# Optimization experiments

Measured on AMD Instinct MI355X. Metric: run time of the kernel, lower is better.

Reference implementation:

```python
import jax, jax.numpy as jnp
import numpy as np

B, C, HW, P = 8, 128, 50176, 128  # batch, channels, flattened spatial, num parcels

def setup_inputs() -> dict:
    key = jax.random.key(0)
    k1, k2 = jax.random.split(key)
    x = jax.random.normal(k1, (B, C, HW), dtype=jnp.float32)
    # 0/1 parcel assignment mask [b, num_parcs, hw]
    parcel_mask_batch = jax.random.randint(k2, (B, P, HW), 0, 2).astype(jnp.float32)
    return {"x": x, "parcel_mask_batch": parcel_mask_batch}

def reference(x, parcel_mask_batch):
    # torch: for each i, x[i] @ mask[i].T  -> stacked [b, c, num_parcs]
    # out[b, c, p] = sum_hw x[b, c, hw] * mask[b, p, hw]
    return jnp.einsum('bch,bph->bcp', x, parcel_mask_batch)
```

## Files before the change

kernel.cpp:

```cpp
#include <hip/hip_runtime.h>
#include <hip/hip_bf16.h>

typedef float f32x4 __attribute__((ext_vector_type(4)));
typedef short short8 __attribute__((ext_vector_type(8)));

#define BATCH 8
#define CH    128
#define HWN   50176
#define PN    128
#define KSPLIT 64
#define KWIN  784
#define BK    64
#define NST   13

__device__ __forceinline__ ushort f2bf(float f){
  uint u = __float_as_uint(f);
  u += 0x7FFFu + ((u >> 16) & 1u);
  return (ushort)(u >> 16);
}
__device__ __forceinline__ float bf2f(ushort h){
  return __uint_as_float(((uint)h) << 16);
}

template<int EPI>
__global__ __launch_bounds__(256, 2)
void raggr_kernel(const float* __restrict__ X, const float* __restrict__ Mk,
                  float* __restrict__ OUT, float* __restrict__ PART){
  __shared__ char lds[49152];
  char* Xh = lds;
  char* Xl = lds + 16384;
  char* Mm = lds + 32768;

  const int tid  = threadIdx.x;
  const int b    = blockIdx.x >> 6;
  const int s    = blockIdx.x & 63;
  const int lane = tid & 63;
  const int wid  = tid >> 6;
  const int wrow = (wid >> 1) * 64;
  const int wcol = (wid & 1) * 64;

  const size_t base = (size_t)b * CH * HWN + (size_t)s * KWIN;
  const f32x4 z4 = {0.f, 0.f, 0.f, 0.f};

  f32x4 acc[4][4];
  #pragma unroll
  for(int m=0;m<4;++m)
    #pragma unroll
    for(int n=0;n<4;++n) acc[m][n] = z4;

  f32x4 xv[8], mv[8];

  #define ISSUE(tt) {                                                         \
    const int kv = (KWIN - (tt)*BK) < BK ? (KWIN - (tt)*BK) : BK;             \
    _Pragma("unroll")                                                         \
    for(int it=0; it<8; ++it){                                                \
      int f = it*256 + tid;                                                   \
      int row = f >> 4, kq = f & 15;                                          \
      bool ok = (kq*4) < kv;                                                  \
      size_t off = base + (size_t)row * HWN + (size_t)((tt)*BK + kq*4);       \
      size_t offc = ok ? off : base;                                          \
      f32x4 xt = *(const f32x4*)(X  + offc);                                  \
      f32x4 mt = *(const f32x4*)(Mk + offc);                                  \
      xv[it] = ok ? xt : z4;                                                  \
      mv[it] = ok ? mt : z4;                                                  \
    } }

  #define WRITE_LDS() {                                                       \
    _Pragma("unroll")                                                         \
    for(int it=0; it<8; ++it){                                                \
      int f = it*256 + tid;                                                   \
      int row = f >> 4, kq = f & 15;                                          \
      int boff = row*128 + ((kq*8) ^ ((row & 7) << 4));                       \
      ushort h0=f2bf(xv[it].x), h1=f2bf(xv[it].y),                            \
             h2=f2bf(xv[it].z), h3=f2bf(xv[it].w);                            \
      ushort l0=f2bf(xv[it].x - bf2f(h0)), l1=f2bf(xv[it].y - bf2f(h1)),      \
             l2=f2bf(xv[it].z - bf2f(h2)), l3=f2bf(xv[it].w - bf2f(h3));      \
      ushort m0=f2bf(mv[it].x), m1=f2bf(mv[it].y),                            \
             m2=f2bf(mv[it].z), m3=f2bf(mv[it].w);                            \
      uint2 uh; uh.x = (uint)h0 | ((uint)h1<<16); uh.y = (uint)h2 | ((uint)h3<<16); \
      uint2 ul; ul.x = (uint)l0 | ((uint)l1<<16); ul.y = (uint)l2 | ((uint)l3<<16); \
      uint2 um; um.x = (uint)m0 | ((uint)m1<<16); um.y = (uint)m2 | ((uint)m3<<16); \
      *(uint2*)(Xh + boff) = uh;                                              \
      *(uint2*)(Xl + boff) = ul;                                              \
      *(uint2*)(Mm + boff) = um;                                              \
    } }

  #define COMPUTE() {                                                         \
    _Pragma("unroll")                                                         \
    for(int ks=0; ks<2; ++ks){                                                \
      const int kb = ks*64 + ((lane >> 4) << 4);                              \
      short8 bfr[4], ah[4], al[4];                                            \
      _Pragma("unroll")                                                       \
      for(int n=0;n<4;++n){                                                   \
        int r = wcol + n*16 + (lane & 15);                                    \
        bfr[n] = *(const short8*)(Mm + r*128 + (kb ^ ((r&7)<<4)));            \
      }                                                                       \
      _Pragma("unroll")                                                       \
      for(int m=0;m<4;++m){                                                   \
        int r = wrow + m*16 + (lane & 15);                                    \
        int o = r*128 + (kb ^ ((r&7)<<4));                                    \
        ah[m] = *(const short8*)(Xh + o);                                     \
        al[m] = *(const short8*)(Xl + o);                                     \
      }                                                                       \
      _Pragma("unroll")                                                       \
      for(int m=0;m<4;++m)                                                    \
        _Pragma("unroll")                                                     \
        for(int n=0;n<4;++n){                                                 \
          acc[m][n] = __builtin_amdgcn_mfma_f32_16x16x32_bf16(ah[m], bfr[n], acc[m][n], 0,0,0); \
          acc[m][n] = __builtin_amdgcn_mfma_f32_16x16x32_bf16(al[m], bfr[n], acc[m][n], 0,0,0); \
        }                                                                     \
    } }

  ISSUE(0);
  WRITE_LDS();
  __syncthreads();

  #pragma unroll 1
  for(int t=0; t<NST; ++t){
    if(t+1 < NST) ISSUE(t+1);
    COMPUTE();
    __syncthreads();
    if(t+1 < NST){ WRITE_LDS(); __syncthreads(); }
  }

  if(EPI == 0){
    float* p = PART + ((size_t)(b*KSPLIT + s)) * 16384;
    #pragma unroll
    for(int m=0;m<4;++m){
      int row0 = wrow + m*16 + ((lane >> 4) << 2);
      #pragma unroll
      for(int n=0;n<4;++n){
        int col = wcol + n*16 + (lane & 15);
        #pragma unroll
        for(int j=0;j<4;++j) p[(size_t)(row0+j)*128 + col] = acc[m][n][j];
      }
    }
  } else {
    float* o = OUT + (size_t)b * 16384;
    #pragma unroll
    for(int m=0;m<4;++m){
      int row0 = wrow + m*16 + ((lane >> 4) << 2);
      #pragma unroll
      for(int n=0;n<4;++n){
        int col = wcol + n*16 + (lane & 15);
        #pragma unroll
        for(int j=0;j<4;++j) atomicAdd(&o[(size_t)(row0+j)*128 + col], acc[m][n][j]);
      }
    }
  }
}

__global__ void reduce_kernel(const float* __restrict__ PART, float* __restrict__ OUT){
  int idx = blockIdx.x * 256 + threadIdx.x;
  int b   = idx >> 12;
  int c4  = idx & 4095;
  const f32x4* p = (const f32x4*)PART;
  f32x4 sum = {0.f,0.f,0.f,0.f};
  size_t base_ = (size_t)b * KSPLIT * 4096 + (size_t)c4;
  #pragma unroll 8
  for(int s2=0; s2<KSPLIT; ++s2) sum += p[base_ + (size_t)s2*4096];
  ((f32x4*)OUT)[idx] = sum;
}

__global__ void zero_kernel(float* __restrict__ OUT){
  int idx = blockIdx.x * 256 + threadIdx.x;
  if(idx < BATCH*CH*PN) OUT[idx] = 0.f;
}

extern "C" void kernel_launch(void* const* d_in, const int* in_sizes, int n_in,
                              void* d_out, int out_size, void* d_ws, size_t ws_size,
                              hipStream_t stream){
  const float* X  = (const float*)d_in[0];
  const float* Mk = (const float*)d_in[1];
  float* O = (float*)d_out;

  const size_t part_bytes = (size_t)BATCH * KSPLIT * CH * PN * sizeof(float);
  if(ws_size >= part_bytes && d_ws != nullptr){
    float* part = (float*)d_ws;
    raggr_kernel<0><<<dim3(BATCH*KSPLIT), dim3(256), 0, stream>>>(X, Mk, O, part);
    reduce_kernel<<<dim3(128), dim3(256), 0, stream>>>(part, O);
  } else {
    zero_kernel<<<dim3(512), dim3(256), 0, stream>>>(O);
    raggr_kernel<1><<<dim3(BATCH*KSPLIT), dim3(256), 0, stream>>>(X, Mk, O, nullptr);
  }
}
```

Before: 428.1 us.

## Stage fp32 tiles via direct global-to-LDS loads with double buffering

Replaces the register-staged load, convert and LDS write path with global_load_lds DMA copies of raw fp32 tiles into double-buffered shared memory, cutting the K tile from 64 to 32 and removing one barrier per step. The bf16 hi/lo split of X and the mask conversion (now truncation) move to after the LDS read, inside the compute phase. A separate tail step handles the leftover 16 columns. This trades redundant per-wave conversion work and doubled fp32 LDS traffic for overlapped, register-free loading.

```diff
diff --git a/kernel.cpp b/kernel.cpp
--- a/kernel.cpp
+++ b/kernel.cpp
@@ -10,37 +10,69 @@
 #define PN    128
 #define KSPLIT 64
 #define KWIN  784
-#define BK    64
-#define NST   13
-
-__device__ __forceinline__ ushort f2bf(float f){
+#define BK    32
+#define NFULL 24
+#define TAILOFF (NFULL*BK)
+
+__device__ __forceinline__ ushort f2bf_rn(float f){
   uint u = __float_as_uint(f);
   u += 0x7FFFu + ((u >> 16) & 1u);
   return (ushort)(u >> 16);
 }
 __device__ __forceinline__ float bf2f(ushort h){
   return __uint_as_float(((uint)h) << 16);
+}
+
+__device__ __forceinline__ short8 cvt8_trunc(f32x4 a, f32x4 b){
+  union{ short8 v; ushort u[8]; } r;
+  r.u[0]=(ushort)(__float_as_uint(a.x)>>16); r.u[1]=(ushort)(__float_as_uint(a.y)>>16);
+  r.u[2]=(ushort)(__float_as_uint(a.z)>>16); r.u[3]=(ushort)(__float_as_uint(a.w)>>16);
+  r.u[4]=(ushort)(__float_as_uint(b.x)>>16); r.u[5]=(ushort)(__float_as_uint(b.y)>>16);
+  r.u[6]=(ushort)(__float_as_uint(b.z)>>16); r.u[7]=(ushort)(__float_as_uint(b.w)>>16);
+  return r.v;
+}
+
+__device__ __forceinline__ void cvt8_hilo(f32x4 a, f32x4 b, short8& h8, short8& l8){
+  union{ short8 v; ushort u[8]; } h, l;
+  float f[8] = {a.x,a.y,a.z,a.w,b.x,b.y,b.z,b.w};
+  #pragma unroll
+  for(int j=0;j<8;++j){
+    ushort hh = f2bf_rn(f[j]);
+    h.u[j] = hh;
+    l.u[j] = f2bf_rn(f[j] - bf2f(hh));
+  }
+  h8 = h.v; l8 = l.v;
+}
+
+__device__ __forceinline__ void gload16(const float* g, float* l){
+  __builtin_amdgcn_global_load_lds(
+      (const __attribute__((address_space(1))) void*)g,
+      (__attribute__((address_space(3))) void*)l, 16, 0, 0);
+}
+
+__device__ __forceinline__ f32x4 lds_read4(const float* base, int r, int slot){
+  return *(const f32x4*)(base + r*32 + ((slot ^ (r&7)) << 2));
+}
+__device__ __forceinline__ void lds_write4(float* base, int r, int slot, f32x4 v){
+  *(f32x4*)(base + r*32 + ((slot ^ (r&7)) << 2)) = v;
 }
 
 template<int EPI>
 __global__ __launch_bounds__(256, 2)
 void raggr_kernel(const float* __restrict__ X, const float* __restrict__ Mk,
                   float* __restrict__ OUT, float* __restrict__ PART){
-  __shared__ char lds[49152];
-  char* Xh = lds;
-  char* Xl = lds + 16384;
-  char* Mm = lds + 32768;
+  __shared__ float lds[2][2][4096];
 
   const int tid  = threadIdx.x;
   const int b    = blockIdx.x >> 6;
   const int s    = blockIdx.x & 63;
   const int lane = tid & 63;
-  const int wid  = tid >> 6;
-  const int wrow = (wid >> 1) * 64;
-  const int wcol = (wid & 1) * 64;
+  const int w    = tid >> 6;
+  const int wrow = (w >> 1) * 64;
+  const int wcol = (w & 1) * 64;
 
   const size_t base = (size_t)b * CH * HWN + (size_t)s * KWIN;
-  const f32x4 z4 = {0.f, 0.f, 0.f, 0.f};
+  const f32x4 z4 = {0.f,0.f,0.f,0.f};
 
   f32x4 acc[4][4];
   #pragma unroll
@@ -48,79 +80,71 @@
     #pragma unroll
     for(int n=0;n<4;++n) acc[m][n] = z4;
 
-  f32x4 xv[8], mv[8];
-
-  #define ISSUE(tt) {                                                         \
-    const int kv = (KWIN - (tt)*BK) < BK ? (KWIN - (tt)*BK) : BK;             \
-    _Pragma("unroll")                                                         \
-    for(int it=0; it<8; ++it){                                                \
-      int f = it*256 + tid;                                                   \
-      int row = f >> 4, kq = f & 15;                                          \
-      bool ok = (kq*4) < kv;                                                  \
-      size_t off = base + (size_t)row * HWN + (size_t)((tt)*BK + kq*4);       \
-      size_t offc = ok ? off : base;                                          \
-      f32x4 xt = *(const f32x4*)(X  + offc);                                  \
-      f32x4 mt = *(const f32x4*)(Mk + offc);                                  \
-      xv[it] = ok ? xt : z4;                                                  \
-      mv[it] = ok ? mt : z4;                                                  \
+  const int lrow = lane >> 3;
+  const int kq   = (lane & 7) ^ lrow;
+  const float* pX[4]; const float* pM[4];
+  #pragma unroll
+  for(int i=0;i<4;++i){
+    int r = w*32 + i*8 + lrow;
+    pX[i] = X  + base + (size_t)r * HWN + kq*4;
+    pM[i] = Mk + base + (size_t)r * HWN + kq*4;
+  }
+
+  #define STAGE(tt, buf) {                                                    \
+    _Pragma("unroll")                                                         \
+    for(int i=0;i<4;++i){                                                     \
+      gload16(pX[i] + (tt)*BK, &lds[buf][0][(w*4+i)*256]);                    \
+      gload16(pM[i] + (tt)*BK, &lds[buf][1][(w*4+i)*256]);                    \
     } }
 
-  #define WRITE_LDS() {                                                       \
-    _Pragma("unroll")                                                         \
-    for(int it=0; it<8; ++it){                                                \
-      int f = it*256 + tid;                                                   \
-      int row = f >> 4, kq = f & 15;                                          \
-      int boff = row*128 + ((kq*8) ^ ((row & 7) << 4));                       \
-      ushort h0=f2bf(xv[it].x), h1=f2bf(xv[it].y),                            \
-             h2=f2bf(xv[it].z), h3=f2bf(xv[it].w);                            \
-      ushort l0=f2bf(xv[it].x - bf2f(h0)), l1=f2bf(xv[it].y - bf2f(h1)),      \
-             l2=f2bf(xv[it].z - bf2f(h2)), l3=f2bf(xv[it].w - bf2f(h3));      \
-      ushort m0=f2bf(mv[it].x), m1=f2bf(mv[it].y),                            \
-             m2=f2bf(mv[it].z), m3=f2bf(mv[it].w);                            \
-      uint2 uh; uh.x = (uint)h0 | ((uint)h1<<16); uh.y = (uint)h2 | ((uint)h3<<16); \
-      uint2 ul; ul.x = (uint)l0 | ((uint)l1<<16); ul.y = (uint)l2 | ((uint)l3<<16); \
-      uint2 um; um.x = (uint)m0 | ((uint)m1<<16); um.y = (uint)m2 | ((uint)m3<<16); \
-      *(uint2*)(Xh + boff) = uh;                                              \
-      *(uint2*)(Xl + boff) = ul;                                              \
-      *(uint2*)(Mm + boff) = um;                                              \
-    } }
-
-  #define COMPUTE() {                                                         \
-    _Pragma("unroll")                                                         \
-    for(int ks=0; ks<2; ++ks){                                                \
-      const int kb = ks*64 + ((lane >> 4) << 4);                              \
-      short8 bfr[4], ah[4], al[4];                                            \
+  #define COMPUTE(buf) {                                                      \
+    const float* Xb = lds[buf][0];                                            \
+    const float* Mb = lds[buf][1];                                            \
+    const int l15 = lane & 15;                                                \
+    const int s0  = (lane >> 4) * 2;                                          \
+    short8 bf[4], ah[4], al[4];                                               \
+    _Pragma("unroll")                                                         \
+    for(int n=0;n<4;++n){                                                     \
+      int r = wcol + n*16 + l15;                                              \
+      bf[n] = cvt8_trunc(lds_read4(Mb, r, s0), lds_read4(Mb, r, s0+1));       \
+    }                                                                         \
+    _Pragma("unroll")                                                         \
+    for(int m=0;m<4;++m){                                                     \
+      int r = wrow + m*16 + l15;                                              \
+      cvt8_hilo(lds_read4(Xb, r, s0), lds_read4(Xb, r, s0+1), ah[m], al[m]);  \
+    }                                                                         \
+    _Pragma("unroll")                                                         \
+    for(int m=0;m<4;++m)                                                      \
       _Pragma("unroll")                                                       \
       for(int n=0;n<4;++n){                                                   \
-        int r = wcol + n*16 + (lane & 15);                                    \
-        bfr[n] = *(const short8*)(Mm + r*128 + (kb ^ ((r&7)<<4)));            \
+        acc[m][n] = __builtin_amdgcn_mfma_f32_16x16x32_bf16(ah[m], bf[n], acc[m][n], 0,0,0); \
+        acc[m][n] = __builtin_amdgcn_mfma_f32_16x16x32_bf16(al[m], bf[n], acc[m][n], 0,0,0); \
       }                                                                       \
-      _Pragma("unroll")                                                       \
-      for(int m=0;m<4;++m){                                                   \
-        int r = wrow + m*16 + (lane & 15);                                    \
-        int o = r*128 + (kb ^ ((r&7)<<4));                                    \
-        ah[m] = *(const short8*)(Xh + o);                                     \
-        al[m] = *(const short8*)(Xl + o);                                     \
-      }                                                                       \
-      _Pragma("unroll")                                                       \
-      for(int m=0;m<4;++m)                                                    \
-        _Pragma("unroll")                                                     \
-        for(int n=0;n<4;++n){                                                 \
-          acc[m][n] = __builtin_amdgcn_mfma_f32_16x16x32_bf16(ah[m], bfr[n], acc[m][n], 0,0,0); \
-          acc[m][n] = __builtin_amdgcn_mfma_f32_16x16x32_bf16(al[m], bfr[n], acc[m][n], 0,0,0); \
-        }                                                                     \
-    } }
-
-  ISSUE(0);
-  WRITE_LDS();
+  }
+
+  STAGE(0, 0);
   __syncthreads();
 
   #pragma unroll 1
-  for(int t=0; t<NST; ++t){
-    if(t+1 < NST) ISSUE(t+1);
-    COMPUTE();
+  for(int t=0; t<NFULL; ++t){
+    if(t+1 < NFULL) STAGE(t+1, (t+1)&1);
+    COMPUTE(t&1);
     __syncthreads();
-    if(t+1 < NST){ WRITE_LDS(); __syncthreads(); }
+  }
+
+  {
+    int r    = tid >> 1;
+    int half = tid & 1;
+    size_t g = base + (size_t)r * HWN + TAILOFF + half*8;
+    f32x4 x0 = *(const f32x4*)(X + g),  x1 = *(const f32x4*)(X + g + 4);
+    f32x4 m0 = *(const f32x4*)(Mk + g), m1 = *(const f32x4*)(Mk + g + 4);
+    float* Xb = lds[0][0]; float* Mb = lds[0][1];
+    lds_write4(Xb, r, half*2,   x0); lds_write4(Xb, r, half*2+1, x1);
+    lds_write4(Xb, r, 4+half*2, z4); lds_write4(Xb, r, 5+half*2, z4);
+    lds_write4(Mb, r, half*2,   m0); lds_write4(Mb, r, half*2+1, m1);
+    lds_write4(Mb, r, 4+half*2, z4); lds_write4(Mb, r, 5+half*2, z4);
+    __syncthreads();
+    COMPUTE(0);
   }
 
   if(EPI == 0){
@@ -148,6 +172,8 @@
       }
     }
   }
+  #undef STAGE
+  #undef COMPUTE
 }
 
 __global__ void reduce_kernel(const float* __restrict__ PART, float* __restrict__ OUT){
```

After: 431.5 us. Within noise of the previous version (+0.8%).
